# Kernel optimization log

Measured on AMD Instinct MI355X. Metric: run time of the kernel, lower is better.

The kernel has to match this reference:

```python
import jax, jax.numpy as jnp
import numpy as np
from jax import lax

TAGSET = 9
START, STOP = 7, 8
HID = 500  # hidden_dim // 2 per direction
BERT_H = 768
T = 8192
NEG = -10000.0


def setup_inputs() -> dict:
    key = jax.random.key(0)
    ks = jax.random.split(key, 16)
    trans = jax.random.normal(ks[13], (TAGSET, TAGSET), jnp.float32)
    trans = trans.at[START, :].set(NEG).at[:, STOP].set(NEG)
    return {
        "embeddings": jax.random.normal(ks[0], (T, BERT_H), jnp.float32),
        "w_ih_f": jax.random.normal(ks[1], (4 * HID, BERT_H), jnp.float32) * 0.05,
        "w_hh_f": jax.random.normal(ks[2], (4 * HID, HID), jnp.float32) * 0.05,
        "b_ih_f": jax.random.normal(ks[3], (4 * HID,), jnp.float32) * 0.05,
        "b_hh_f": jax.random.normal(ks[4], (4 * HID,), jnp.float32) * 0.05,
        "w_ih_b": jax.random.normal(ks[5], (4 * HID, BERT_H), jnp.float32) * 0.05,
        "w_hh_b": jax.random.normal(ks[6], (4 * HID, HID), jnp.float32) * 0.05,
        "b_ih_b": jax.random.normal(ks[7], (4 * HID,), jnp.float32) * 0.05,
        "b_hh_b": jax.random.normal(ks[8], (4 * HID,), jnp.float32) * 0.05,
        "h0": jax.random.normal(ks[9], (2, HID), jnp.float32),
        "c0": jax.random.normal(ks[10], (2, HID), jnp.float32),
        "w_tag": jax.random.normal(ks[11], (TAGSET, 2 * HID), jnp.float32) * 0.05,
        "b_tag": jax.random.normal(ks[12], (TAGSET,), jnp.float32) * 0.05,
        "transitions": trans,
    }


def _lstm_dir(x, w_ih, w_hh, b_ih, b_hh, h0, c0, reverse):
    # pre-compute input projections for all timesteps: [T, 4H]
    xproj = x @ w_ih.T + b_ih + b_hh

    def step(carry, xp):
        h, c = carry
        g = xp + w_hh @ h  # [4H]
        i, f, gg, o = jnp.split(g, 4)  # torch gate order: i, f, g, o
        i, f, o = jax.nn.sigmoid(i), jax.nn.sigmoid(f), jax.nn.sigmoid(o)
        c = f * c + i * jnp.tanh(gg)
        h = o * jnp.tanh(c)
        return (h, c), h

    _, hs = lax.scan(step, (h0, c0), xproj, reverse=reverse)
    return hs  # [T, H]


def _viterbi(feats, transitions):
    init = jnp.full((TAGSET,), NEG, feats.dtype).at[START].set(0.0)

    def step(fv, feat):
        scores = fv[None, :] + transitions  # [next_tag, prev_tag]
        bptr = jnp.argmax(scores, axis=1)
        fv_new = jnp.max(scores, axis=1) + feat
        return fv_new, bptr

    fv, bptrs = lax.scan(step, init, feats)  # bptrs: [T, TAGSET]
    terminal = fv + transitions[STOP]
    best_last = jnp.argmax(terminal)
    path_score = terminal[best_last]

    def back(tag, bp):
        return bp[tag], tag  # emit tag at time t, carry tag at t-1

    _, path = lax.scan(back, best_last, bptrs, reverse=True)
    return path_score, path


def reference(embeddings, w_ih_f, w_hh_f, b_ih_f, b_hh_f,
              w_ih_b, w_hh_b, b_ih_b, b_hh_b,
              h0, c0, w_tag, b_tag, transitions):
    h_fwd = _lstm_dir(embeddings, w_ih_f, w_hh_f, b_ih_f, b_hh_f, h0[0], c0[0], False)
    h_bwd = _lstm_dir(embeddings, w_ih_b, w_hh_b, b_ih_b, b_hh_b, h0[1], c0[1], True)
    lstm_out = jnp.concatenate([h_fwd, h_bwd], axis=-1)  # [T, 1000]
    feats = lstm_out @ w_tag.T + b_tag  # [T, TAGSET]
    score, path = _viterbi(feats, transitions)
    return score, path
```

## Files before the change

### kernel.cpp

```cpp
#include <hip/hip_runtime.h>
#include <hip/hip_bf16.h>
#include <math.h>

constexpr int TSEQ = 8192;
constexpr int BH   = 768;
constexpr int HID  = 500;
constexpr int H4   = 2000;
constexpr int NTAG = 9;
constexpr int START_TAG = 7;
constexpr int STOP_TAG  = 8;
constexpr float NEGV = -10000.0f;

constexpr int NWG = 32;
constexpr int UPW = 16;
constexpr int LSTM_BLOCKS = 2 * NWG;
constexpr int TOTAL_BLOCKS = 256;

constexpr size_t XP_OFF = 0;
constexpr size_t XP_SZ  = (size_t)2 * TSEQ * H4;
constexpr size_t HS_OFF = XP_OFF + XP_SZ;
constexpr size_t HS_SZ  = (size_t)2 * TSEQ * HID;
constexpr size_t FT_OFF = HS_OFF + HS_SZ;
constexpr size_t FT_SZ  = (size_t)TSEQ * NTAG;
constexpr size_t BUF_OFF = FT_OFF + FT_SZ;

__device__ __forceinline__ float wave_reduce_sum(float v) {
    int x;
    x = __builtin_amdgcn_update_dpp(0, __float_as_int(v), 0x111, 0xF, 0xF, true);
    v += __int_as_float(x);
    x = __builtin_amdgcn_update_dpp(0, __float_as_int(v), 0x112, 0xF, 0xF, true);
    v += __int_as_float(x);
    x = __builtin_amdgcn_update_dpp(0, __float_as_int(v), 0x114, 0xF, 0xF, true);
    v += __int_as_float(x);
    x = __builtin_amdgcn_update_dpp(0, __float_as_int(v), 0x118, 0xF, 0xF, true);
    v += __int_as_float(x);
    x = __builtin_amdgcn_update_dpp(0, __float_as_int(v), 0x142, 0xF, 0xF, true);
    v += __int_as_float(x);
    x = __builtin_amdgcn_update_dpp(0, __float_as_int(v), 0x143, 0xF, 0xF, true);
    v += __int_as_float(x);
    return v;
}

__device__ __forceinline__ float fast_sigmoid(float x) {
    return __builtin_amdgcn_rcpf(1.f + __expf(-x));
}
__device__ __forceinline__ float fast_tanh(float x) {
    const float xc = fminf(fmaxf(x, -15.f), 15.f);
    const float e = __expf(2.f * xc);
    return (e - 1.f) * __builtin_amdgcn_rcpf(e + 1.f);
}

__global__ __launch_bounds__(256) void xproj_gemm(
    const float* __restrict__ A,
    const float* __restrict__ Wf, const float* __restrict__ Wb,
    const float* __restrict__ bif, const float* __restrict__ bhf,
    const float* __restrict__ bib, const float* __restrict__ bhb,
    float* __restrict__ out)
{
    __shared__ __align__(16) float As[8 * 128];
    __shared__ __align__(16) float Bs[8 * 128];

    const int bx = blockIdx.x, by = blockIdx.y;
    const int d    = by >> 4;
    const int col0 = (by & 15) << 7;
    const int row0 = bx << 7;
    const float* W  = d ? Wb : Wf;
    const float* bi = d ? bib : bif;
    const float* bh = d ? bhb : bhf;

    const int tid = threadIdx.x;
    const int tx = tid & 15, ty = tid >> 4;

    float acc[8][8];
#pragma unroll
    for (int i = 0; i < 8; ++i)
#pragma unroll
        for (int j = 0; j < 8; ++j) acc[i][j] = 0.f;

    const int lm = tid >> 1;
    const int lk = (tid & 1) << 2;
    const float* Ap = A + (size_t)(row0 + lm) * BH + lk;
    const int wcol = col0 + lm;
    const bool wok = wcol < H4;
    const float* Wp = W + (size_t)(wok ? wcol : 0) * BH + lk;

    for (int k0 = 0; k0 < BH; k0 += 8) {
        const float4 av = *(const float4*)(Ap + k0);
        float4 bv = make_float4(0.f, 0.f, 0.f, 0.f);
        if (wok) bv = *(const float4*)(Wp + k0);
        __syncthreads();
        As[(lk + 0) * 128 + lm] = av.x;
        As[(lk + 1) * 128 + lm] = av.y;
        As[(lk + 2) * 128 + lm] = av.z;
        As[(lk + 3) * 128 + lm] = av.w;
        Bs[(lk + 0) * 128 + lm] = bv.x;
        Bs[(lk + 1) * 128 + lm] = bv.y;
        Bs[(lk + 2) * 128 + lm] = bv.z;
        Bs[(lk + 3) * 128 + lm] = bv.w;
        __syncthreads();
#pragma unroll
        for (int kk = 0; kk < 8; ++kk) {
            float a[8], b[8];
            *(float4*)&a[0] = *(const float4*)&As[kk * 128 + ty * 8];
            *(float4*)&a[4] = *(const float4*)&As[kk * 128 + ty * 8 + 4];
            *(float4*)&b[0] = *(const float4*)&Bs[kk * 128 + tx * 8];
            *(float4*)&b[4] = *(const float4*)&Bs[kk * 128 + tx * 8 + 4];
#pragma unroll
            for (int i = 0; i < 8; ++i)
#pragma unroll
                for (int j = 0; j < 8; ++j)
                    acc[i][j] = fmaf(a[i], b[j], acc[i][j]);
        }
    }

#pragma unroll
    for (int i = 0; i < 8; ++i) {
        const int r = row0 + ty * 8 + i;
#pragma unroll
        for (int j = 0; j < 8; ++j) {
            const int cc = col0 + tx * 8 + j;
            if (cc < H4)
                out[((size_t)d * TSEQ + r) * H4 + cc] = acc[i][j] + bi[cc] + bh[cc];
        }
    }
}

__global__ __launch_bounds__(512) void lstm_rec(
    const float* __restrict__ whhf, const float* __restrict__ whhb,
    const float* __restrict__ h0, const float* __restrict__ c0,
    const float* __restrict__ xproj_all, float* __restrict__ hseq_all,
    unsigned long long* bufbase)
{
    __shared__ __align__(16) float wlds[64 * 512];
    __shared__ __align__(16) float hs[512];
    __shared__ float gparts[64];

    const int bx = blockIdx.x;
    const int tid = threadIdx.x, l = tid & 63, wv = tid >> 6;

    if (bx >= LSTM_BLOCKS) {
        const unsigned long long* t0 = bufbase;
        const unsigned long long* t1 = bufbase + 1024;
        float a0 = 1.0f + (float)tid * 1e-6f;
        float a1 = 1.1f, a2 = 1.2f, a3 = 1.3f;
        const float m = 0.999999f, c = 1e-7f;
        for (;;) {
#pragma unroll 8
            for (int it = 0; it < 512; ++it) {
                a0 = fmaf(a0, m, c); a1 = fmaf(a1, m, c);
                a2 = fmaf(a2, m, c); a3 = fmaf(a3, m, c);
            }
            asm volatile("" : "+v"(a0), "+v"(a1), "+v"(a2), "+v"(a3));
            const unsigned long long v0 =
                __hip_atomic_load(t0, __ATOMIC_RELAXED, __HIP_MEMORY_SCOPE_AGENT);
            const unsigned long long v1 =
                __hip_atomic_load(t1, __ATOMIC_RELAXED, __HIP_MEMORY_SCOPE_AGENT);
            if ((v0 >> 32) == (unsigned)TSEQ && (v1 >> 32) == (unsigned)TSEQ)
                break;
        }
        return;
    }

    const int d = bx & 1, w = bx >> 1;
    const float* whh = d ? whhb : whhf;
    const float* xproj = xproj_all + (size_t)d * TSEQ * H4;
    float* hseq = hseq_all + (size_t)d * TSEQ * HID;
    unsigned long long* bufd = bufbase + d * 1024;

    const int j0 = w * UPW;
    int nu = HID - j0; if (nu > UPW) nu = UPW; if (nu < 0) nu = 0;

    for (int idx = tid; idx < 64 * 512; idx += 512) {
        const int r = idx >> 9, c = idx & 511;
        const int g = r >> 4, u = r & 15;
        float vv = 0.f;
        if (c < HID && u < nu)
            vv = whh[(size_t)(g * HID + j0 + u) * HID + c];
        wlds[idx] = vv;
    }
    float creg = 0.f;
    if (tid < nu) {
        creg = c0[d * HID + j0 + tid];
        const unsigned long long pk =
            (unsigned long long)__float_as_uint(h0[d * HID + j0 + tid]);
        __hip_atomic_store(&bufd[j0 + tid], pk,
                           __ATOMIC_RELAXED, __HIP_MEMORY_SCOPE_AGENT);
    }
    __syncthreads();

    const int ua = 4 * l, ub = 256 + 4 * l;
    const bool gb0 = (ub + 0 >= HID), gb1 = (ub + 1 >= HID);
    const bool gb2 = (ub + 2 >= HID), gb3 = (ub + 3 >= HID);

    for (int step = 0; step < TSEQ; ++step) {
        const int t = d ? (TSEQ - 1 - step) : step;

        float xp0 = 0.f, xp1 = 0.f, xp2 = 0.f, xp3 = 0.f;
        if (tid < nu) {
            const float* xr = xproj + (size_t)t * H4 + j0 + tid;
            xp0 = xr[0]; xp1 = xr[HID]; xp2 = xr[2 * HID]; xp3 = xr[3 * HID];
        }

        if (wv == 0) {
            unsigned long long* bp = bufd + ((step & 1) << 9);
            const unsigned long long want = (unsigned long long)(unsigned)step;
            unsigned long long va0, va1, va2, va3, vb0, vb1, vb2, vb3;
            for (;;) {
                va0 = __hip_atomic_load(&bp[ua + 0], __ATOMIC_RELAXED, __HIP_MEMORY_SCOPE_AGENT);
                va1 = __hip_atomic_load(&bp[ua + 1], __ATOMIC_RELAXED, __HIP_MEMORY_SCOPE_AGENT);
                va2 = __hip_atomic_load(&bp[ua + 2], __ATOMIC_RELAXED, __HIP_MEMORY_SCOPE_AGENT);
                va3 = __hip_atomic_load(&bp[ua + 3], __ATOMIC_RELAXED, __HIP_MEMORY_SCOPE_AGENT);
                vb0 = __hip_atomic_load(&bp[ub + 0], __ATOMIC_RELAXED, __HIP_MEMORY_SCOPE_AGENT);
                vb1 = __hip_atomic_load(&bp[ub + 1], __ATOMIC_RELAXED, __HIP_MEMORY_SCOPE_AGENT);
                vb2 = __hip_atomic_load(&bp[ub + 2], __ATOMIC_RELAXED, __HIP_MEMORY_SCOPE_AGENT);
                vb3 = __hip_atomic_load(&bp[ub + 3], __ATOMIC_RELAXED, __HIP_MEMORY_SCOPE_AGENT);
                bool ok = true;
                ok &= ((va0 >> 32) == want);
                ok &= ((va1 >> 32) == want);
                ok &= ((va2 >> 32) == want);
                ok &= ((va3 >> 32) == want);
                ok &= gb0 || ((vb0 >> 32) == want);
                ok &= gb1 || ((vb1 >> 32) == want);
                ok &= gb2 || ((vb2 >> 32) == want);
                ok &= gb3 || ((vb3 >> 32) == want);
                if (__all(ok)) break;
            }
            float4 fa, fb;
            fa.x = __uint_as_float((unsigned)va0);
            fa.y = __uint_as_float((unsigned)va1);
            fa.z = __uint_as_float((unsigned)va2);
            fa.w = __uint_as_float((unsigned)va3);
            fb.x = __uint_as_float((unsigned)vb0);
            fb.y = __uint_as_float((unsigned)vb1);
            fb.z = __uint_as_float((unsigned)vb2);
            fb.w = __uint_as_float((unsigned)vb3);
            *(float4*)&hs[ua] = fa;
            *(float4*)&hs[ub] = fb;
        }
        __syncthreads();

        const float4 ha = *(const float4*)&hs[ua];
        const float4 hb = *(const float4*)&hs[ub];
#pragma unroll
        for (int r8 = 0; r8 < 8; ++r8) {
            const int row = (wv << 3) + r8;
            const float4 w0 = *(const float4*)&wlds[(row << 9) + ua];
            const float4 w1 = *(const float4*)&wlds[(row << 9) + ub];
            float p = w0.x * ha.x + w0.y * ha.y + w0.z * ha.z + w0.w * ha.w
                    + w1.x * hb.x + w1.y * hb.y + w1.z * hb.z + w1.w * hb.w;
            p = wave_reduce_sum(p);
            if (l == 63) gparts[row] = p;
        }
        __syncthreads();

        if (tid < nu) {
            const float gi = gparts[tid]      + xp0;
            const float gf = gparts[16 + tid] + xp1;
            const float gg = gparts[32 + tid] + xp2;
            const float go = gparts[48 + tid] + xp3;
            const float si = fast_sigmoid(gi);
            const float sf = fast_sigmoid(gf);
            const float so = fast_sigmoid(go);
            const float c = sf * creg + si * fast_tanh(gg);
            creg = c;
            const float h = so * fast_tanh(c);
            const unsigned long long pk =
                ((unsigned long long)(unsigned)(step + 1) << 32) | __float_as_uint(h);
            __hip_atomic_store(&bufd[(((step + 1) & 1) << 9) + j0 + tid], pk,
                               __ATOMIC_RELAXED, __HIP_MEMORY_SCOPE_AGENT);
            hseq[(size_t)t * HID + j0 + tid] = h;
        }
    }
}

__global__ __launch_bounds__(256) void feats_kern(
    const float* __restrict__ hsf, const float* __restrict__ hsb,
    const float* __restrict__ wtag, const float* __restrict__ btag,
    float* __restrict__ feats)
{
    __shared__ float wt[NTAG * 1000];
    __shared__ float bt[NTAG];
    const int tid = threadIdx.x;
    for (int idx = tid; idx < NTAG * 1000; idx += 256) wt[idx] = wtag[idx];
    if (tid < NTAG) bt[tid] = btag[tid];
    __syncthreads();

    const int t = blockIdx.x * 4 + (tid >> 6);
    const int l = tid & 63;
    float acc[NTAG];
#pragma unroll
    for (int n = 0; n < NTAG; ++n) acc[n] = 0.f;

#pragma unroll
    for (int j = 0; j < 16; ++j) {
        const int k = l + 64 * j;
        if (k < 1000) {
            const float a = (k < HID) ? hsf[(size_t)t * HID + k]
                                      : hsb[(size_t)t * HID + k - HID];
#pragma unroll
            for (int n = 0; n < NTAG; ++n)
                acc[n] = fmaf(wt[n * 1000 + k], a, acc[n]);
        }
    }
#pragma unroll
    for (int n = 0; n < NTAG; ++n) {
        acc[n] += __shfl_xor(acc[n], 1, 64);
        acc[n] += __shfl_xor(acc[n], 2, 64);
        acc[n] += __shfl_xor(acc[n], 4, 64);
        acc[n] += __shfl_xor(acc[n], 8, 64);
        acc[n] += __shfl_xor(acc[n], 16, 64);
        acc[n] += __shfl_xor(acc[n], 32, 64);
    }
    if (l < NTAG) feats[(size_t)t * NTAG + l] = acc[l] + bt[l];
}

__global__ __launch_bounds__(256) void viterbi_kern(
    const float* __restrict__ feats, const float* __restrict__ trans,
    float* __restrict__ out)
{
    __shared__ unsigned char bp[TSEQ * NTAG];
    __shared__ float fch[512 * NTAG];
    __shared__ __align__(16) float fvL[12];
    __shared__ unsigned char amap[256];
    __shared__ unsigned char entry[32];
    __shared__ int s_best;

    const int tid = threadIdx.x, l = tid & 63, wv = tid >> 6;
    const int ln = (l < NTAG) ? l : NTAG - 1;
    float tr[NTAG];
#pragma unroll
    for (int p = 0; p < NTAG; ++p) tr[p] = trans[ln * NTAG + p];

    if (tid < 12) fvL[tid] = (tid == START_TAG) ? 0.f : NEGV;
    __syncthreads();

    for (int c = 0; c < 16; ++c) {
        for (int idx = tid; idx < 512 * NTAG; idx += 256)
            fch[idx] = feats[(size_t)c * 512 * NTAG + idx];
        __syncthreads();
        if (wv == 0) {
            for (int tt = 0; tt < 512; ++tt) {
                const float ft = fch[tt * NTAG + ln];
                const float4 f0 = *(const float4*)&fvL[0];
                const float4 f1 = *(const float4*)&fvL[4];
                const float f8 = fvL[8];
                const float c0 = f0.x + tr[0];
                const float c1 = f0.y + tr[1];
                const float c2 = f0.z + tr[2];
                const float c3 = f0.w + tr[3];
                const float c4 = f1.x + tr[4];
                const float c5 = f1.y + tr[5];
                const float c6 = f1.z + tr[6];
                const float c7 = f1.w + tr[7];
                const float c8 = f8   + tr[8];
                const float m0 = fmaxf(fmaxf(c0, c1), c2);
                const float m1 = fmaxf(fmaxf(c3, c4), c5);
                const float m2 = fmaxf(fmaxf(c6, c7), c8);
                const float best = fmaxf(fmaxf(m0, m1), m2);
                unsigned m = (c0 == best ? 1u : 0u)
                           | (c1 == best ? 2u : 0u)
                           | (c2 == best ? 4u : 0u)
                           | (c3 == best ? 8u : 0u)
                           | (c4 == best ? 16u : 0u)
                           | (c5 == best ? 32u : 0u)
                           | (c6 == best ? 64u : 0u)
                           | (c7 == best ? 128u : 0u)
                           | (c8 == best ? 256u : 0u);
                const int b = __builtin_ctz(m);
                const float nf = best + ft;
                if (l < NTAG) {
                    bp[(size_t)(c * 512 + tt) * NTAG + l] = (unsigned char)b;
                    fvL[l] = nf;
                }
            }
        }
        __syncthreads();
    }

    if (tid == 0) {
        float bestv = -3.0e38f; int bi = 0;
#pragma unroll
        for (int p = 0; p < NTAG; ++p) {
            const float s = fvL[p] + trans[STOP_TAG * NTAG + p];
            if (s > bestv) { bestv = s; bi = p; }
        }
        out[0] = bestv; s_best = bi;
    }
    __syncthreads();

    if (tid < 252) {
        const int ch = tid / 9, tg = tid % 9;
        const int s = ch * 293;
        const int e = (s + 293 < TSEQ) ? s + 293 : TSEQ;
        int tag = tg;
        for (int t = e - 1; t >= s; --t) tag = bp[t * NTAG + tag];
        amap[ch * 9 + tg] = (unsigned char)tag;
    }
    __syncthreads();
    if (tid == 0) {
        int tag = s_best;
        entry[27] = (unsigned char)tag;
        for (int ch = 27; ch >= 1; --ch) {
            tag = amap[ch * 9 + tag];
            entry[ch - 1] = (unsigned char)tag;
        }
    }
    __syncthreads();
    if (tid < 28) {
        const int ch = tid;
        const int s = ch * 293;
        const int e = (s + 293 < TSEQ) ? s + 293 : TSEQ;
        int tag = entry[ch];
        for (int t = e - 1; t >= s; --t) {
            out[1 + t] = (float)tag;
            tag = bp[t * NTAG + tag];
        }
    }
}

extern "C" void kernel_launch(void* const* d_in, const int* in_sizes, int n_in,
                              void* d_out, int out_size, void* d_ws, size_t ws_size,
                              hipStream_t stream) {
    const float* emb  = (const float*)d_in[0];
    const float* wihf = (const float*)d_in[1];
    const float* whhf = (const float*)d_in[2];
    const float* bihf = (const float*)d_in[3];
    const float* bhhf = (const float*)d_in[4];
    const float* wihb = (const float*)d_in[5];
    const float* whhb = (const float*)d_in[6];
    const float* bihb = (const float*)d_in[7];
    const float* bhhb = (const float*)d_in[8];
    const float* h0   = (const float*)d_in[9];
    const float* c0   = (const float*)d_in[10];
    const float* wtag = (const float*)d_in[11];
    const float* btag = (const float*)d_in[12];
    const float* trans = (const float*)d_in[13];

    float* ws = (float*)d_ws;
    float* out = (float*)d_out;

    xproj_gemm<<<dim3(64, 32), 256, 0, stream>>>(
        emb, wihf, wihb, bihf, bhhf, bihb, bhhb, ws + XP_OFF);

    lstm_rec<<<TOTAL_BLOCKS, 512, 0, stream>>>(
        whhf, whhb, h0, c0, ws + XP_OFF, ws + HS_OFF,
        (unsigned long long*)(ws + BUF_OFF));

    feats_kern<<<TSEQ / 4, 256, 0, stream>>>(
        ws + HS_OFF, ws + HS_OFF + (size_t)TSEQ * HID, wtag, btag, ws + FT_OFF);

    viterbi_kern<<<1, 256, 0, stream>>>(ws + FT_OFF, trans, out);
}
```

Measured before the change: 18.05 ms.

## Interleave forward and backward LSTM directions within each block with prefetched polling

Each LSTM block now handles 8 hidden units of both directions instead of 16 units of one direction, alternating forward and backward steps. This lets the wait for one direction's h broadcast overlap with the other direction's compute. Polling loads for the next direction's buffer are issued before they are needed, so the spin usually finds the data already present. The block count drops from 64 to 63 and the number of __syncthreads per step doubles. Each direction's step now also waits behind the other direction's work in the same block.

After: 25.59 ms. +41.7%, slower.

```diff
diff --git a/kernel.cpp b/kernel.cpp
--- a/kernel.cpp
+++ b/kernel.cpp
@@ -11,9 +11,8 @@
 constexpr int STOP_TAG  = 8;
 constexpr float NEGV = -10000.0f;
 
-constexpr int NWG = 32;
-constexpr int UPW = 16;
-constexpr int LSTM_BLOCKS = 2 * NWG;
+constexpr int UPW = 8;
+constexpr int LSTM_BLOCKS = 63;
 constexpr int TOTAL_BLOCKS = 256;
 
 constexpr size_t XP_OFF = 0;
@@ -50,6 +49,9 @@
     return (e - 1.f) * __builtin_amdgcn_rcpf(e + 1.f);
 }
 
+#define ALD(p) __hip_atomic_load((p), __ATOMIC_RELAXED, __HIP_MEMORY_SCOPE_AGENT)
+#define AST(p, v) __hip_atomic_store((p), (v), __ATOMIC_RELAXED, __HIP_MEMORY_SCOPE_AGENT)
+
 __global__ __launch_bounds__(256) void xproj_gemm(
     const float* __restrict__ A,
     const float* __restrict__ Wf, const float* __restrict__ Wb,
@@ -131,9 +133,12 @@
     const float* __restrict__ xproj_all, float* __restrict__ hseq_all,
     unsigned long long* bufbase)
 {
-    __shared__ __align__(16) float wlds[64 * 512];
-    __shared__ __align__(16) float hs[512];
-    __shared__ float gparts[64];
+    __shared__ __align__(16) float wldsF[32 * 512];
+    __shared__ __align__(16) float wldsB[32 * 512];
+    __shared__ __align__(16) float hsF[512];
+    __shared__ __align__(16) float hsB[512];
+    __shared__ float gpF[32];
+    __shared__ float gpB[32];
 
     const int bx = blockIdx.x;
     const int tid = threadIdx.x, l = tid & 63, wv = tid >> 6;
@@ -151,40 +156,42 @@
                 a2 = fmaf(a2, m, c); a3 = fmaf(a3, m, c);
             }
             asm volatile("" : "+v"(a0), "+v"(a1), "+v"(a2), "+v"(a3));
-            const unsigned long long v0 =
-                __hip_atomic_load(t0, __ATOMIC_RELAXED, __HIP_MEMORY_SCOPE_AGENT);
-            const unsigned long long v1 =
-                __hip_atomic_load(t1, __ATOMIC_RELAXED, __HIP_MEMORY_SCOPE_AGENT);
+            const unsigned long long v0 = ALD(t0);
+            const unsigned long long v1 = ALD(t1);
             if ((v0 >> 32) == (unsigned)TSEQ && (v1 >> 32) == (unsigned)TSEQ)
                 break;
         }
         return;
     }
 
-    const int d = bx & 1, w = bx >> 1;
-    const float* whh = d ? whhb : whhf;
-    const float* xproj = xproj_all + (size_t)d * TSEQ * H4;
-    float* hseq = hseq_all + (size_t)d * TSEQ * HID;
-    unsigned long long* bufd = bufbase + d * 1024;
-
-    const int j0 = w * UPW;
+    const int j0 = bx * UPW;
     int nu = HID - j0; if (nu > UPW) nu = UPW; if (nu < 0) nu = 0;
 
-    for (int idx = tid; idx < 64 * 512; idx += 512) {
+    const float* xprF = xproj_all;
+    const float* xprB = xproj_all + (size_t)TSEQ * H4;
+    float* hsqF = hseq_all;
+    float* hsqB = hseq_all + (size_t)TSEQ * HID;
+    unsigned long long* bufF = bufbase;
+    unsigned long long* bufB = bufbase + 1024;
+
+    for (int idx = tid; idx < 32 * 512; idx += 512) {
         const int r = idx >> 9, c = idx & 511;
-        const int g = r >> 4, u = r & 15;
-        float vv = 0.f;
-        if (c < HID && u < nu)
-            vv = whh[(size_t)(g * HID + j0 + u) * HID + c];
-        wlds[idx] = vv;
-    }
-    float creg = 0.f;
+        const int g = r >> 3, u = r & 7;
+        float vf = 0.f, vb = 0.f;
+        if (c < HID && u < nu) {
+            const size_t off = (size_t)(g * HID + j0 + u) * HID + c;
+            vf = whhf[off];
+            vb = whhb[off];
+        }
+        wldsF[idx] = vf;
+        wldsB[idx] = vb;
+    }
+    float cregF = 0.f, cregB = 0.f;
     if (tid < nu) {
-        creg = c0[d * HID + j0 + tid];
-        const unsigned long long pk =
-            (unsigned long long)__float_as_uint(h0[d * HID + j0 + tid]);
-        __hip_atomic_store(&bufd[j0 + tid], pk,
-                           __ATOMIC_RELAXED, __HIP_MEMORY_SCOPE_AGENT);
+        cregF = c0[j0 + tid];
+        cregB = c0[HID + j0 + tid];
+        AST(&bufF[j0 + tid], (unsigned long long)__float_as_uint(h0[j0 + tid]));
+        AST(&bufB[j0 + tid], (unsigned long long)__float_as_uint(h0[HID + j0 + tid]));
     }
     __syncthreads();
 
@@ -192,83 +199,162 @@
     const bool gb0 = (ub + 0 >= HID), gb1 = (ub + 1 >= HID);
     const bool gb2 = (ub + 2 >= HID), gb3 = (ub + 3 >= HID);
 
+    unsigned long long pFa0=0,pFa1=0,pFa2=0,pFa3=0,pFb0=0,pFb1=0,pFb2=0,pFb3=0;
+    unsigned long long pBa0=0,pBa1=0,pBa2=0,pBa3=0,pBb0=0,pBb1=0,pBb2=0,pBb3=0;
+    if (wv == 0) {
+        pFa0 = ALD(&bufF[ua + 0]); pFa1 = ALD(&bufF[ua + 1]);
+        pFa2 = ALD(&bufF[ua + 2]); pFa3 = ALD(&bufF[ua + 3]);
+        pFb0 = ALD(&bufF[ub + 0]); pFb1 = ALD(&bufF[ub + 1]);
+        pFb2 = ALD(&bufF[ub + 2]); pFb3 = ALD(&bufF[ub + 3]);
+    }
+
     for (int step = 0; step < TSEQ; ++step) {
-        const int t = d ? (TSEQ - 1 - step) : step;
-
-        float xp0 = 0.f, xp1 = 0.f, xp2 = 0.f, xp3 = 0.f;
+        float xf0=0,xf1=0,xf2=0,xf3=0, xb0=0,xb1=0,xb2=0,xb3=0;
         if (tid < nu) {
-            const float* xr = xproj + (size_t)t * H4 + j0 + tid;
-            xp0 = xr[0]; xp1 = xr[HID]; xp2 = xr[2 * HID]; xp3 = xr[3 * HID];
+            const float* xrF = xprF + (size_t)step * H4 + j0 + tid;
+            xf0 = xrF[0]; xf1 = xrF[HID]; xf2 = xrF[2 * HID]; xf3 = xrF[3 * HID];
+            const float* xrB = xprB + (size_t)(TSEQ - 1 - step) * H4 + j0 + tid;
+            xb0 = xrB[0]; xb1 = xrB[HID]; xb2 = xrB[2 * HID]; xb3 = xrB[3 * HID];
         }
 
         if (wv == 0) {
-            unsigned long long* bp = bufd + ((step & 1) << 9);
+            unsigned long long* bp = bufF + ((step & 1) << 9);
             const unsigned long long want = (unsigned long long)(unsigned)step;
-            unsigned long long va0, va1, va2, va3, vb0, vb1, vb2, vb3;
             for (;;) {
-                va0 = __hip_atomic_load(&bp[ua + 0], __ATOMIC_RELAXED, __HIP_MEMORY_SCOPE_AGENT);
-                va1 = __hip_atomic_load(&bp[ua + 1], __ATOMIC_RELAXED, __HIP_MEMORY_SCOPE_AGENT);
-                va2 = __hip_atomic_load(&bp[ua + 2], __ATOMIC_RELAXED, __HIP_MEMORY_SCOPE_AGENT);
-                va3 = __hip_atomic_load(&bp[ua + 3], __ATOMIC_RELAXED, __HIP_MEMORY_SCOPE_AGENT);
-                vb0 = __hip_atomic_load(&bp[ub + 0], __ATOMIC_RELAXED, __HIP_MEMORY_SCOPE_AGENT);
-                vb1 = __hip_atomic_load(&bp[ub + 1], __ATOMIC_RELAXED, __HIP_MEMORY_SCOPE_AGENT);
-                vb2 = __hip_atomic_load(&bp[ub + 2], __ATOMIC_RELAXED, __HIP_MEMORY_SCOPE_AGENT);
-                vb3 = __hip_atomic_load(&bp[ub + 3], __ATOMIC_RELAXED, __HIP_MEMORY_SCOPE_AGENT);
-                bool ok = true;
-                ok &= ((va0 >> 32) == want);
-                ok &= ((va1 >> 32) == want);
-                ok &= ((va2 >> 32) == want);
-                ok &= ((va3 >> 32) == want);
-                ok &= gb0 || ((vb0 >> 32) == want);
-                ok &= gb1 || ((vb1 >> 32) == want);
-                ok &= gb2 || ((vb2 >> 32) == want);
-                ok &= gb3 || ((vb3 >> 32) == want);
+                bool ok = ((pFa0 >> 32) == want)
+                        & ((pFa1 >> 32) == want)
+                        & ((pFa2 >> 32) == want)
+                        & ((pFa3 >> 32) == want)
+                        & (gb0 | ((pFb0 >> 32) == want))
+                        & (gb1 | ((pFb1 >> 32) == want))
+                        & (gb2 | ((pFb2 >> 32) == want))
+                        & (gb3 | ((pFb3 >> 32) == want));
                 if (__all(ok)) break;
+                pFa0 = ALD(&bp[ua + 0]); pFa1 = ALD(&bp[ua + 1]);
+                pFa2 = ALD(&bp[ua + 2]); pFa3 = ALD(&bp[ua + 3]);
+                pFb0 = ALD(&bp[ub + 0]); pFb1 = ALD(&bp[ub + 1]);
+                pFb2 = ALD(&bp[ub + 2]); pFb3 = ALD(&bp[ub + 3]);
             }
             float4 fa, fb;
-            fa.x = __uint_as_float((unsigned)va0);
-            fa.y = __uint_as_float((unsigned)va1);
-            fa.z = __uint_as_float((unsigned)va2);
-            fa.w = __uint_as_float((unsigned)va3);
-            fb.x = __uint_as_float((unsigned)vb0);
-            fb.y = __uint_as_float((unsigned)vb1);
-            fb.z = __uint_as_float((unsigned)vb2);
-            fb.w = __uint_as_float((unsigned)vb3);
-            *(float4*)&hs[ua] = fa;
-            *(float4*)&hs[ub] = fb;
-        }
-        __syncthreads();
-
-        const float4 ha = *(const float4*)&hs[ua];
-        const float4 hb = *(const float4*)&hs[ub];
-#pragma unroll
-        for (int r8 = 0; r8 < 8; ++r8) {
-            const int row = (wv << 3) + r8;
-            const float4 w0 = *(const float4*)&wlds[(row << 9) + ua];
-            const float4 w1 = *(const float4*)&wlds[(row << 9) + ub];
-            float p = w0.x * ha.x + w0.y * ha.y + w0.z * ha.z + w0.w * ha.w
-                    + w1.x * hb.x + w1.y * hb.y + w1.z * hb.z + w1.w * hb.w;
-            p = wave_reduce_sum(p);
-            if (l == 63) gparts[row] = p;
+            fa.x = __uint_as_float((unsigned)pFa0);
+            fa.y = __uint_as_float((unsigned)pFa1);
+            fa.z = __uint_as_float((unsigned)pFa2);
+            fa.w = __uint_as_float((unsigned)pFa3);
+            fb.x = __uint_as_float((unsigned)pFb0);
+            fb.y = __uint_as_float((unsigned)pFb1);
+            fb.z = __uint_as_float((unsigned)pFb2);
+            fb.w = __uint_as_float((unsigned)pFb3);
+            *(float4*)&hsF[ua] = fa;
+            *(float4*)&hsF[ub] = fb;
+            unsigned long long* nbp = bufB + ((step & 1) << 9);
+            pBa0 = ALD(&nbp[ua + 0]); pBa1 = ALD(&nbp[ua + 1]);
+            pBa2 = ALD(&nbp[ua + 2]); pBa3 = ALD(&nbp[ua + 3]);
+            pBb0 = ALD(&nbp[ub + 0]); pBb1 = ALD(&nbp[ub + 1]);
+            pBb2 = ALD(&nbp[ub + 2]); pBb3 = ALD(&nbp[ub + 3]);
+        }
+        __syncthreads();
+
+        {
+            const float4 ha = *(const float4*)&hsF[ua];
+            const float4 hb = *(const float4*)&hsF[ub];
+#pragma unroll
+            for (int k = 0; k < 4; ++k) {
+                const int row = (wv << 2) + k;
+                const float4 w0 = *(const float4*)&wldsF[(row << 9) + ua];
+                const float4 w1 = *(const float4*)&wldsF[(row << 9) + ub];
+                float p = w0.x * ha.x + w0.y * ha.y + w0.z * ha.z + w0.w * ha.w
+                        + w1.x * hb.x + w1.y * hb.y + w1.z * hb.z + w1.w * hb.w;
+                p = wave_reduce_sum(p);
+                if (l == 63) gpF[row] = p;
+            }
         }
         __syncthreads();
 
         if (tid < nu) {
-            const float gi = gparts[tid]      + xp0;
-            const float gf = gparts[16 + tid] + xp1;
-            const float gg = gparts[32 + tid] + xp2;
-            const float go = gparts[48 + tid] + xp3;
+            const float gi = gpF[tid]      + xf0;
+            const float gf = gpF[8 + tid]  + xf1;
+            const float gg = gpF[16 + tid] + xf2;
+            const float go = gpF[24 + tid] + xf3;
             const float si = fast_sigmoid(gi);
             const float sf = fast_sigmoid(gf);
             const float so = fast_sigmoid(go);
-            const float c = sf * creg + si * fast_tanh(gg);
-            creg = c;
+            const float c = sf * cregF + si * fast_tanh(gg);
+            cregF = c;
             const float h = so * fast_tanh(c);
             const unsigned long long pk =
                 ((unsigned long long)(unsigned)(step + 1) << 32) | __float_as_uint(h);
-            __hip_atomic_store(&bufd[(((step + 1) & 1) << 9) + j0 + tid], pk,
-                               __ATOMIC_RELAXED, __HIP_MEMORY_SCOPE_AGENT);
-            hseq[(size_t)t * HID + j0 + tid] = h;
+            AST(&bufF[(((step + 1) & 1) << 9) + j0 + tid], pk);
+            hsqF[(size_t)step * HID + j0 + tid] = h;
+        }
+
+        if (wv == 0) {
+            unsigned long long* bp = bufB + ((step & 1) << 9);
+            const unsigned long long want = (unsigned long long)(unsigned)step;
+            for (;;) {
+                bool ok = ((pBa0 >> 32) == want)
+                        & ((pBa1 >> 32) == want)
+                        & ((pBa2 >> 32) == want)
+                        & ((pBa3 >> 32) == want)
+                        & (gb0 | ((pBb0 >> 32) == want))
+                        & (gb1 | ((pBb1 >> 32) == want))
+                        & (gb2 | ((pBb2 >> 32) == want))
+                        & (gb3 | ((pBb3 >> 32) == want));
+                if (__all(ok)) break;
+                pBa0 = ALD(&bp[ua + 0]); pBa1 = ALD(&bp[ua + 1]);
+                pBa2 = ALD(&bp[ua + 2]); pBa3 = ALD(&bp[ua + 3]);
+                pBb0 = ALD(&bp[ub + 0]); pBb1 = ALD(&bp[ub + 1]);
+                pBb2 = ALD(&bp[ub + 2]); pBb3 = ALD(&bp[ub + 3]);
+            }
+            float4 fa, fb;
+            fa.x = __uint_as_float((unsigned)pBa0);
+            fa.y = __uint_as_float((unsigned)pBa1);
+            fa.z = __uint_as_float((unsigned)pBa2);
+            fa.w = __uint_as_float((unsigned)pBa3);
+            fb.x = __uint_as_float((unsigned)pBb0);
+            fb.y = __uint_as_float((unsigned)pBb1);
+            fb.z = __uint_as_float((unsigned)pBb2);
+            fb.w = __uint_as_float((unsigned)pBb3);
+            *(float4*)&hsB[ua] = fa;
+            *(float4*)&hsB[ub] = fb;
+            unsigned long long* nbp = bufF + (((step + 1) & 1) << 9);
+            pFa0 = ALD(&nbp[ua + 0]); pFa1 = ALD(&nbp[ua + 1]);
+            pFa2 = ALD(&nbp[ua + 2]); pFa3 = ALD(&nbp[ua + 3]);
+            pFb0 = ALD(&nbp[ub + 0]); pFb1 = ALD(&nbp[ub + 1]);
+            pFb2 = ALD(&nbp[ub + 2]); pFb3 = ALD(&nbp[ub + 3]);
+        }
+        __syncthreads();
+
+        {
+            const float4 ha = *(const float4*)&hsB[ua];
+            const float4 hb = *(const float4*)&hsB[ub];
+#pragma unroll
+            for (int k = 0; k < 4; ++k) {
+                const int row = (wv << 2) + k;
+                const float4 w0 = *(const float4*)&wldsB[(row << 9) + ua];
+                const float4 w1 = *(const float4*)&wldsB[(row << 9) + ub];
+                float p = w0.x * ha.x + w0.y * ha.y + w0.z * ha.z + w0.w * ha.w
+                        + w1.x * hb.x + w1.y * hb.y + w1.z * hb.z + w1.w * hb.w;
+                p = wave_reduce_sum(p);
+                if (l == 63) gpB[row] = p;
+            }
+        }
+        __syncthreads();
+
+        if (tid < nu) {
+            const float gi = gpB[tid]      + xb0;
+            const float gf = gpB[8 + tid]  + xb1;
+            const float gg = gpB[16 + tid] + xb2;
+            const float go = gpB[24 + tid] + xb3;
+            const float si = fast_sigmoid(gi);
+            const float sf = fast_sigmoid(gf);
+            const float so = fast_sigmoid(go);
+            const float c = sf * cregB + si * fast_tanh(gg);
+            cregB = c;
+            const float h = so * fast_tanh(c);
+            const unsigned long long pk =
+                ((unsigned long long)(unsigned)(step + 1) << 32) | __float_as_uint(h);
+            AST(&bufB[(((step + 1) & 1) << 9) + j0 + tid], pk);
+            hsqB[(size_t)(TSEQ - 1 - step) * HID + j0 + tid] = h;
         }
     }
 }
```
